# Optimization experiments

Measured on AMD Instinct MI355X. Metric: run time of the kernel, lower is better.

Reference implementation:

```python
import jax, jax.numpy as jnp
import numpy as np

EPS = 1e-5

def _conv(x, w, pad):
    # NCHW / OIHW 2-D convolution, stride 1
    return jax.lax.conv_general_dilated(
        x, w, window_strides=(1, 1), padding=[(pad, pad), (pad, pad)],
        dimension_numbers=('NCHW', 'OIHW', 'NCHW'))

def _bn2d(x, g, b, m, v):
    inv = g * jax.lax.rsqrt(v + EPS)
    return x * inv[None, :, None, None] + (b - m * inv)[None, :, None, None]

def _bn1d(x, g, b, m, v):
    inv = g * jax.lax.rsqrt(v + EPS)
    return x * inv[None, :] + (b - m * inv)[None, :]

def _avgpool2(x):
    B, C, H, W = x.shape
    return x.reshape(B, C, H // 2, 2, W // 2, 2).mean(axis=(3, 5))

def _hardtanh01(x):
    return jnp.clip(x, 0.0, 1.0)

def setup_inputs() -> dict:
    key = jax.random.key(0)
    ks = jax.random.split(key, 24)
    B = 1024
    d = {}
    d['x_in'] = jax.random.normal(ks[0], (B, 3, 32, 32), dtype=jnp.float32)
    d['w1'] = jax.random.normal(ks[1], (32, 3, 5, 5), dtype=jnp.float32) * 0.1
    d['w2'] = jax.random.normal(ks[2], (32, 32, 5, 5), dtype=jnp.float32) * 0.05
    d['w3'] = jax.random.normal(ks[3], (64, 32, 5, 5), dtype=jnp.float32) * 0.05
    d['w4'] = jax.random.normal(ks[4], (10, 64, 4, 4), dtype=jnp.float32) * 0.05
    for i, (c, k0) in enumerate([(32, 5), (32, 9), (64, 13), (10, 17)], start=1):
        d[f'g{i}'] = jax.random.uniform(ks[k0], (c,), minval=0.5, maxval=1.5, dtype=jnp.float32)
        d[f'b{i}'] = jax.random.normal(ks[k0 + 1], (c,), dtype=jnp.float32) * 0.1
        d[f'm{i}'] = jax.random.normal(ks[k0 + 2], (c,), dtype=jnp.float32) * 0.1
        d[f'v{i}'] = jax.random.uniform(ks[k0 + 3], (c,), minval=0.5, maxval=1.5, dtype=jnp.float32)
    return d

def reference(x_in, w1, w2, w3, w4,
              g1, b1, m1, v1, g2, b2, m2, v2,
              g3, b3, m3, v3, g4, b4, m4, v4):
    # conv1 -> bn1 -> pool -> hardtanh(0,1)
    x = _hardtanh01(_avgpool2(_bn2d(_conv(x_in, w1, 2), g1, b1, m1, v1)))
    # conv2 -> bn2 -> pool -> hardtanh(0,1)
    x = _hardtanh01(_avgpool2(_bn2d(_conv(x, w2, 2), g2, b2, m2, v2)))
    # conv3 -> bn3 -> pool -> hardtanh(0,1)
    x = _hardtanh01(_avgpool2(_bn2d(_conv(x, w3, 2), g3, b3, m3, v3)))
    # fc1 as 4x4 conv, valid padding -> (B, num_classes, 1, 1)
    x = _conv(x, w4, 0).reshape(x.shape[0], -1)
    return _bn1d(x, g4, b4, m4, v4)
```

## Files before the change

### kernel.cpp

```cpp
#include <hip/hip_runtime.h>

#define EPSF 1e-5f

typedef _Float16 half8 __attribute__((ext_vector_type(8)));
typedef _Float16 half4v __attribute__((ext_vector_type(4)));
typedef _Float16 half2v __attribute__((ext_vector_type(2)));
typedef float f32x4 __attribute__((ext_vector_type(4)));

__device__ __forceinline__ float clamp01(float x){ return fminf(fmaxf(x, 0.f), 1.f); }

__global__ __launch_bounds__(256) void k_prep(
    const float* __restrict__ w1, const float* __restrict__ w2,
    const float* __restrict__ w3, const float* __restrict__ w4,
    const float* __restrict__ g1, const float* __restrict__ b1, const float* __restrict__ m1, const float* __restrict__ v1,
    const float* __restrict__ g2, const float* __restrict__ b2, const float* __restrict__ m2, const float* __restrict__ v2,
    const float* __restrict__ g3, const float* __restrict__ b3, const float* __restrict__ m3, const float* __restrict__ v3,
    const float* __restrict__ g4, const float* __restrict__ b4, const float* __restrict__ m4, const float* __restrict__ v4,
    _Float16* __restrict__ w1h, _Float16* __restrict__ w2h, _Float16* __restrict__ w3h,
    _Float16* __restrict__ w4h, float* __restrict__ bnc)
{
  const int t = blockIdx.x*256 + threadIdx.x;
  if (t < 5120) {
    int c = t / 160, k = t - c*160;
    int oc = (c < 16) ? 2*c : 2*(c-16)+1;
    int dy = k >> 5, rem = k & 31, dx = rem >> 2, ic = rem & 3;
    float val = (dx < 5 && ic < 3) ? w1[(oc*3+ic)*25 + dy*5 + dx] : 0.f;
    w1h[t] = (_Float16)val;
  }
  for (int i = t; i < 25600; i += 32768) {
    int tap = i >> 10, r = i & 1023, c = r >> 5, ic = r & 31;
    int oc = (c < 16) ? 2*c : 2*(c-16)+1;
    w2h[i] = (_Float16)w2[(oc*32+ic)*25 + tap];
  }
  for (int i = t; i < 51200; i += 32768) {
    int tap = i >> 11, r = i & 2047, oc = r >> 5, ic = r & 31;
    w3h[i] = (_Float16)w3[(oc*32+ic)*25 + tap];
  }
  for (int i = t; i < 16384; i += 32768) {
    int oc = i >> 10, k = i & 1023, pos = k >> 6, ic = k & 63;
    float val = (oc < 10) ? w4[(oc*64+ic)*16 + pos] : 0.f;
    w4h[i] = (_Float16)val;
  }
  if (t < 32) {
    float inv = g1[t] / sqrtf(v1[t] + EPSF);
    bnc[t] = 0.25f*inv; bnc[32+t] = b1[t] - m1[t]*inv;
    float i2 = g2[t] / sqrtf(v2[t] + EPSF);
    bnc[64+t] = 0.25f*i2; bnc[96+t] = b2[t] - m2[t]*i2;
  }
  if (t < 64) {
    float i3 = g3[t] / sqrtf(v3[t] + EPSF);
    bnc[128+t] = 0.25f*i3; bnc[192+t] = b3[t] - m3[t]*i3;
  }
  if (t < 10) {
    float i4 = g4[t] / sqrtf(v4[t] + EPSF);
    bnc[256+t] = i4; bnc[266+t] = b4[t] - m4[t]*i4;
  }
}

__global__ __launch_bounds__(256, 4) void k_fused(
    const float* __restrict__ x,
    const _Float16* __restrict__ w1h, const _Float16* __restrict__ w2h,
    const _Float16* __restrict__ w3h, const _Float16* __restrict__ w4h,
    const float* __restrict__ bnc, float* __restrict__ out)
{
  __shared__ __align__(16) char arena[32000];
  _Float16* Bx1 = (_Float16*)arena;
  float*    Img = (float*)(arena + 11264);
  _Float16* P2  = (_Float16*)arena;
  _Float16* P3  = (_Float16*)arena;
  _Float16* Ip3 = (_Float16*)(arena + 11520);
  float*    S4P = (float*)(arena + 13568);

  const int img = blockIdx.x;
  const int tid = threadIdx.x;
  const int w   = __builtin_amdgcn_readfirstlane(tid >> 6);
  const int l   = tid & 63;
  const int row = l & 15;
  const int kg  = l >> 4;

  {
    const float4* src = (const float4*)(x + img*3072);
    float4* dst = (float4*)Img;
    dst[tid] = src[tid]; dst[tid+256] = src[tid+256]; dst[tid+512] = src[tid+512];
  }
  __syncthreads();

  for (int j = tid; j < 1400; j += 256) {
    int y = j / 40, xx = j - y*40;
    float s0 = 0.f, s1 = 0.f, s2 = 0.f;
    #pragma unroll
    for (int r = 0; r < 2; ++r) {
      int iy = y - 2 + r;
      if ((unsigned)iy < 32u) {
        #pragma unroll
        for (int cc = 0; cc < 2; ++cc) {
          int ix = xx - 2 + cc;
          if ((unsigned)ix < 32u) {
            const float* ip = Img + iy*32 + ix;
            s0 += ip[0]; s1 += ip[1024]; s2 += ip[2048];
          }
        }
      }
    }
    half4v h; h[0] = (_Float16)s0; h[1] = (_Float16)s1; h[2] = (_Float16)s2; h[3] = (_Float16)0.f;
    *(half4v*)(Bx1 + y*160 + xx*4) = h;
  }
  __syncthreads();

  f32x4 acc1[4][2];
  {
    half8 B1[5][2];
    #pragma unroll
    for (int dy = 0; dy < 5; ++dy) {
      B1[dy][0] = *(const half8*)(w1h + row*160 + dy*32 + kg*8);
      B1[dy][1] = *(const half8*)(w1h + (16 + row)*160 + dy*32 + kg*8);
    }
    #pragma unroll
    for (int mt = 0; mt < 4; ++mt) { acc1[mt][0] = (f32x4){0,0,0,0}; acc1[mt][1] = (f32x4){0,0,0,0}; }
    const int xoff = 8*(row + kg);
    #pragma unroll
    for (int mt = 0; mt < 4; ++mt) {
      const int py = w*4 + mt;
      #pragma unroll
      for (int dy = 0; dy < 5; ++dy) {
        half8 av = *(const half8*)(Bx1 + (2*py + dy)*160 + xoff);
        acc1[mt][0] = __builtin_amdgcn_mfma_f32_16x16x32_f16(av, B1[dy][0], acc1[mt][0], 0, 0, 0);
        acc1[mt][1] = __builtin_amdgcn_mfma_f32_16x16x32_f16(av, B1[dy][1], acc1[mt][1], 0, 0, 0);
      }
    }
  }
  __syncthreads();

  for (int j = tid; j < 1600; j += 256) {
    int u = j & 3, pos = j >> 2;
    int a = pos/20, c = pos - a*20;
    bool interior = ((unsigned)(a-2) < 16u) & ((unsigned)(c-2) < 16u);
    if (!interior) *(half8*)(P2 + pos*40 + u*8) = (half8)(_Float16)0.f;
  }
  {
    const int oce = 2*row;
    const float sA = bnc[oce],   hA = bnc[32 + oce];
    const float sB = bnc[oce+1], hB = bnc[32 + oce + 1];
    #pragma unroll
    for (int mt = 0; mt < 4; ++mt) {
      const int py = w*4 + mt;
      #pragma unroll
      for (int r = 0; r < 4; ++r) {
        int pcol = kg*4 + r;
        int idx = ((py+2)*20 + pcol+2)*40;
        half2v h;
        h[0] = (_Float16)clamp01(fmaf(acc1[mt][0][r], sA, hA));
        h[1] = (_Float16)clamp01(fmaf(acc1[mt][1][r], sB, hB));
        *(half2v*)(P2 + idx + oce) = h;
      }
    }
  }
  __syncthreads();

  f32x4 a2_0 = {0,0,0,0}, a2_1 = {0,0,0,0};
  {
    const int pixel = w*16 + row;
    const int py = pixel >> 3, px = pixel & 7;
    const _Float16* base = P2 + ((2*py)*20 + 2*px)*40 + kg*8;
    half8 RA[6], RB[6];
    #pragma unroll
    for (int c = 0; c < 6; ++c) RA[c] = *(const half8*)(base + c*40);
    #pragma unroll
    for (int c = 0; c < 6; ++c) RB[c] = *(const half8*)(base + 800 + c*40);
    const _Float16* wb = w2h + row*32 + kg*8;
    half8 cw0 = *(const half8*)(wb);
    half8 cw1 = *(const half8*)(wb + 512);
    #pragma unroll
    for (int dy = 0; dy < 5; ++dy) {
      half8 cs[6];
      #pragma unroll
      for (int c = 0; c < 6; ++c) cs[c] = RA[c] + RB[c];
      if (dy < 4) {
        #pragma unroll
        for (int c = 0; c < 6; ++c) {
          half8 nv = *(const half8*)(base + (dy+2)*800 + c*40);
          if ((dy & 1) == 0) RA[c] = nv; else RB[c] = nv;
        }
      }
      #pragma unroll
      for (int dx = 0; dx < 5; ++dx) {
        const int tap = dy*5 + dx;
        const int tn = (tap < 24) ? tap + 1 : 24;
        half8 nw0 = *(const half8*)(wb + tn*1024);
        half8 nw1 = *(const half8*)(wb + tn*1024 + 512);
        half8 av = cs[dx] + cs[dx+1];
        a2_0 = __builtin_amdgcn_mfma_f32_16x16x32_f16(av, cw0, a2_0, 0, 0, 0);
        a2_1 = __builtin_amdgcn_mfma_f32_16x16x32_f16(av, cw1, a2_1, 0, 0, 0);
        cw0 = nw0; cw1 = nw1;
      }
    }
  }
  __syncthreads();

  for (int j = tid; j < 576; j += 256) {
    int u = j & 3, pos = j >> 2;
    int a = pos/12, c = pos - a*12;
    bool interior = ((unsigned)(a-2) < 8u) & ((unsigned)(c-2) < 8u);
    if (!interior) *(half8*)(P3 + pos*40 + u*8) = (half8)(_Float16)0.f;
  }
  {
    const int oce = 2*row;
    const float sA = bnc[64 + oce],   hA = bnc[96 + oce];
    const float sB = bnc[64 + oce+1], hB = bnc[96 + oce + 1];
    #pragma unroll
    for (int r = 0; r < 4; ++r) {
      int p2 = w*16 + kg*4 + r;
      int py2 = p2 >> 3, px2 = p2 & 7;
      int idx = ((py2+2)*12 + px2+2)*40;
      half2v h;
      h[0] = (_Float16)clamp01(fmaf(a2_0[r], sA, hA));
      h[1] = (_Float16)clamp01(fmaf(a2_1[r], sB, hB));
      *(half2v*)(P3 + idx + oce) = h;
    }
  }
  __syncthreads();

  {
    const int py = row >> 2, px = row & 3;
    const _Float16* base = P3 + ((2*py)*12 + 2*px)*40 + kg*8;
    half8 RA[6], RB[6];
    #pragma unroll
    for (int c = 0; c < 6; ++c) RA[c] = *(const half8*)(base + c*40);
    #pragma unroll
    for (int c = 0; c < 6; ++c) RB[c] = *(const half8*)(base + 480 + c*40);
    const _Float16* wb = w3h + (w*16 + row)*32 + kg*8;
    half8 cw = *(const half8*)(wb);
    f32x4 a3 = {0,0,0,0};
    #pragma unroll
    for (int dy = 0; dy < 5; ++dy) {
      half8 cs[6];
      #pragma unroll
      for (int c = 0; c < 6; ++c) cs[c] = RA[c] + RB[c];
      if (dy < 4) {
        #pragma unroll
        for (int c = 0; c < 6; ++c) {
          half8 nv = *(const half8*)(base + (dy+2)*480 + c*40);
          if ((dy & 1) == 0) RA[c] = nv; else RB[c] = nv;
        }
      }
      #pragma unroll
      for (int dx = 0; dx < 5; ++dx) {
        const int tap = dy*5 + dx;
        const int tn = (tap < 24) ? tap + 1 : 24;
        half8 nw = *(const half8*)(wb + tn*2048);
        half8 av = cs[dx] + cs[dx+1];
        a3 = __builtin_amdgcn_mfma_f32_16x16x32_f16(av, cw, a3, 0, 0, 0);
        cw = nw;
      }
    }
    const int oc = w*16 + row;
    const float s3 = bnc[128 + oc], h3 = bnc[192 + oc];
    #pragma unroll
    for (int r = 0; r < 4; ++r)
      Ip3[(kg*4 + r)*64 + oc] = (_Float16)clamp01(fmaf(a3[r], s3, h3));
  }
  __syncthreads();

  if (tid < 160) {
    const int oc = tid >> 4, pix = tid & 15;
    const _Float16* A = Ip3 + pix*64;
    const _Float16* W = w4h + oc*1024 + pix*64;
    float a = 0.f;
    #pragma unroll
    for (int q = 0; q < 8; ++q) {
      half8 xa = *(const half8*)(A + q*8);
      half8 wv = *(const half8*)(W + q*8);
      #pragma unroll
      for (int j = 0; j < 8; ++j)
        a = fmaf((float)xa[j], (float)wv[j], a);
    }
    S4P[tid] = a;
  }
  __syncthreads();
  if (tid < 10) {
    float s = 0.f;
    #pragma unroll
    for (int i = 0; i < 16; ++i) s += S4P[tid*16 + i];
    out[img*10 + tid] = fmaf(s, bnc[256 + tid], bnc[266 + tid]);
  }
}

extern "C" void kernel_launch(void* const* d_in, const int* in_sizes, int n_in,
                              void* d_out, int out_size, void* d_ws, size_t ws_size,
                              hipStream_t stream)
{
  const float* x  = (const float*)d_in[0];
  const float* w1 = (const float*)d_in[1];
  const float* w2 = (const float*)d_in[2];
  const float* w3 = (const float*)d_in[3];
  const float* w4 = (const float*)d_in[4];
  const float *g1=(const float*)d_in[5],  *b1=(const float*)d_in[6],
              *m1=(const float*)d_in[7],  *v1=(const float*)d_in[8];
  const float *g2=(const float*)d_in[9],  *b2=(const float*)d_in[10],
              *m2=(const float*)d_in[11], *v2=(const float*)d_in[12];
  const float *g3=(const float*)d_in[13], *b3=(const float*)d_in[14],
              *m3=(const float*)d_in[15], *v3=(const float*)d_in[16];
  const float *g4=(const float*)d_in[17], *b4=(const float*)d_in[18],
              *m4=(const float*)d_in[19], *v4=(const float*)d_in[20];
  float* out = (float*)d_out;

  char* ws = (char*)d_ws;
  _Float16* w1h = (_Float16*)(ws);
  _Float16* w2h = (_Float16*)(ws + 10240);
  _Float16* w3h = (_Float16*)(ws + 61440);
  _Float16* w4h = (_Float16*)(ws + 163840);
  float*    bnc = (float*)   (ws + 196608);

  k_prep<<<dim3(128), dim3(256), 0, stream>>>(w1, w2, w3, w4,
      g1,b1,m1,v1, g2,b2,m2,v2, g3,b3,m3,v3, g4,b4,m4,v4,
      w1h, w2h, w3h, w4h, bnc);
  k_fused<<<dim3(1024), dim3(256), 0, stream>>>(x, w1h, w2h, w3h, w4h, bnc, out);
}
```

Measured before the change: 126.9 us.

## Split fused conv kernel across eight waves by output-channel halves

The block grows from 256 to 512 threads so the first two conv stages split work two ways across waves. Waves 0-3 and 4-7 each compute one half of the output channels, so each wave issues half the MFMAs and holds half the accumulators. Each wave now writes single fp16 values instead of packed half2 pairs. The third stage still runs only on the first four waves, so those waves are idle on the others while the block keeps more threads and LDS live per image.

```diff
diff --git a/kernel.cpp b/kernel.cpp
--- a/kernel.cpp
+++ b/kernel.cpp
@@ -4,7 +4,6 @@
 
 typedef _Float16 half8 __attribute__((ext_vector_type(8)));
 typedef _Float16 half4v __attribute__((ext_vector_type(4)));
-typedef _Float16 half2v __attribute__((ext_vector_type(2)));
 typedef float f32x4 __attribute__((ext_vector_type(4)));
 
 __device__ __forceinline__ float clamp01(float x){ return fminf(fmaxf(x, 0.f), 1.f); }
@@ -57,7 +56,7 @@
   }
 }
 
-__global__ __launch_bounds__(256, 4) void k_fused(
+__global__ __launch_bounds__(512, 6) void k_fused(
     const float* __restrict__ x,
     const _Float16* __restrict__ w1h, const _Float16* __restrict__ w2h,
     const _Float16* __restrict__ w3h, const _Float16* __restrict__ w4h,
@@ -77,15 +76,18 @@
   const int l   = tid & 63;
   const int row = l & 15;
   const int kg  = l >> 4;
+  const int mtb = w & 3;
+  const int ntb = w >> 2;
 
   {
     const float4* src = (const float4*)(x + img*3072);
     float4* dst = (float4*)Img;
-    dst[tid] = src[tid]; dst[tid+256] = src[tid+256]; dst[tid+512] = src[tid+512];
-  }
-  __syncthreads();
-
-  for (int j = tid; j < 1400; j += 256) {
+    dst[tid] = src[tid];
+    if (tid < 256) dst[tid + 512] = src[tid + 512];
+  }
+  __syncthreads();
+
+  for (int j = tid; j < 1400; j += 512) {
     int y = j / 40, xx = j - y*40;
     float s0 = 0.f, s1 = 0.f, s2 = 0.f;
     #pragma unroll
@@ -107,59 +109,52 @@
   }
   __syncthreads();
 
-  f32x4 acc1[4][2];
-  {
-    half8 B1[5][2];
-    #pragma unroll
-    for (int dy = 0; dy < 5; ++dy) {
-      B1[dy][0] = *(const half8*)(w1h + row*160 + dy*32 + kg*8);
-      B1[dy][1] = *(const half8*)(w1h + (16 + row)*160 + dy*32 + kg*8);
-    }
-    #pragma unroll
-    for (int mt = 0; mt < 4; ++mt) { acc1[mt][0] = (f32x4){0,0,0,0}; acc1[mt][1] = (f32x4){0,0,0,0}; }
+  f32x4 acc1[4];
+  {
+    half8 B1[5];
+    #pragma unroll
+    for (int dy = 0; dy < 5; ++dy)
+      B1[dy] = *(const half8*)(w1h + (ntb*16 + row)*160 + dy*32 + kg*8);
+    #pragma unroll
+    for (int mt = 0; mt < 4; ++mt) acc1[mt] = (f32x4){0,0,0,0};
     const int xoff = 8*(row + kg);
     #pragma unroll
     for (int mt = 0; mt < 4; ++mt) {
-      const int py = w*4 + mt;
+      const int py = mtb*4 + mt;
       #pragma unroll
       for (int dy = 0; dy < 5; ++dy) {
         half8 av = *(const half8*)(Bx1 + (2*py + dy)*160 + xoff);
-        acc1[mt][0] = __builtin_amdgcn_mfma_f32_16x16x32_f16(av, B1[dy][0], acc1[mt][0], 0, 0, 0);
-        acc1[mt][1] = __builtin_amdgcn_mfma_f32_16x16x32_f16(av, B1[dy][1], acc1[mt][1], 0, 0, 0);
-      }
-    }
-  }
-  __syncthreads();
-
-  for (int j = tid; j < 1600; j += 256) {
+        acc1[mt] = __builtin_amdgcn_mfma_f32_16x16x32_f16(av, B1[dy], acc1[mt], 0, 0, 0);
+      }
+    }
+  }
+  __syncthreads();
+
+  for (int j = tid; j < 1600; j += 512) {
     int u = j & 3, pos = j >> 2;
     int a = pos/20, c = pos - a*20;
     bool interior = ((unsigned)(a-2) < 16u) & ((unsigned)(c-2) < 16u);
     if (!interior) *(half8*)(P2 + pos*40 + u*8) = (half8)(_Float16)0.f;
   }
   {
-    const int oce = 2*row;
-    const float sA = bnc[oce],   hA = bnc[32 + oce];
-    const float sB = bnc[oce+1], hB = bnc[32 + oce + 1];
+    const int oc = 2*row + ntb;
+    const float sA = bnc[oc], hA = bnc[32 + oc];
     #pragma unroll
     for (int mt = 0; mt < 4; ++mt) {
-      const int py = w*4 + mt;
+      const int py = mtb*4 + mt;
       #pragma unroll
       for (int r = 0; r < 4; ++r) {
         int pcol = kg*4 + r;
         int idx = ((py+2)*20 + pcol+2)*40;
-        half2v h;
-        h[0] = (_Float16)clamp01(fmaf(acc1[mt][0][r], sA, hA));
-        h[1] = (_Float16)clamp01(fmaf(acc1[mt][1][r], sB, hB));
-        *(half2v*)(P2 + idx + oce) = h;
-      }
-    }
-  }
-  __syncthreads();
-
-  f32x4 a2_0 = {0,0,0,0}, a2_1 = {0,0,0,0};
-  {
-    const int pixel = w*16 + row;
+        P2[idx + oc] = (_Float16)clamp01(fmaf(acc1[mt][r], sA, hA));
+      }
+    }
+  }
+  __syncthreads();
+
+  f32x4 a2 = {0,0,0,0};
+  {
+    const int pixel = mtb*16 + row;
     const int py = pixel >> 3, px = pixel & 7;
     const _Float16* base = P2 + ((2*py)*20 + 2*px)*40 + kg*8;
     half8 RA[6], RB[6];
@@ -167,9 +162,8 @@
     for (int c = 0; c < 6; ++c) RA[c] = *(const half8*)(base + c*40);
     #pragma unroll
     for (int c = 0; c < 6; ++c) RB[c] = *(const half8*)(base + 800 + c*40);
-    const _Float16* wb = w2h + row*32 + kg*8;
-    half8 cw0 = *(const half8*)(wb);
-    half8 cw1 = *(const half8*)(wb + 512);
+    const _Float16* wb = w2h + (ntb*16 + row)*32 + kg*8;
+    half8 cw = *(const half8*)(wb);
     #pragma unroll
     for (int dy = 0; dy < 5; ++dy) {
       half8 cs[6];
@@ -186,41 +180,35 @@
       for (int dx = 0; dx < 5; ++dx) {
         const int tap = dy*5 + dx;
         const int tn = (tap < 24) ? tap + 1 : 24;
-        half8 nw0 = *(const half8*)(wb + tn*1024);
-        half8 nw1 = *(const half8*)(wb + tn*1024 + 512);
+        half8 nw = *(const half8*)(wb + tn*1024);
         half8 av = cs[dx] + cs[dx+1];
-        a2_0 = __builtin_amdgcn_mfma_f32_16x16x32_f16(av, cw0, a2_0, 0, 0, 0);
-        a2_1 = __builtin_amdgcn_mfma_f32_16x16x32_f16(av, cw1, a2_1, 0, 0, 0);
-        cw0 = nw0; cw1 = nw1;
-      }
-    }
-  }
-  __syncthreads();
-
-  for (int j = tid; j < 576; j += 256) {
+        a2 = __builtin_amdgcn_mfma_f32_16x16x32_f16(av, cw, a2, 0, 0, 0);
+        cw = nw;
+      }
+    }
+  }
+  __syncthreads();
+
+  for (int j = tid; j < 576; j += 512) {
     int u = j & 3, pos = j >> 2;
     int a = pos/12, c = pos - a*12;
     bool interior = ((unsigned)(a-2) < 8u) & ((unsigned)(c-2) < 8u);
     if (!interior) *(half8*)(P3 + pos*40 + u*8) = (half8)(_Float16)0.f;
   }
   {
-    const int oce = 2*row;
-    const float sA = bnc[64 + oce],   hA = bnc[96 + oce];
-    const float sB = bnc[64 + oce+1], hB = bnc[96 + oce + 1];
+    const int oc = 2*row + ntb;
+    const float sA = bnc[64 + oc], hA = bnc[96 + oc];
     #pragma unroll
     for (int r = 0; r < 4; ++r) {
-      int p2 = w*16 + kg*4 + r;
+      int p2 = mtb*16 + kg*4 + r;
       int py2 = p2 >> 3, px2 = p2 & 7;
       int idx = ((py2+2)*12 + px2+2)*40;
-      half2v h;
-      h[0] = (_Float16)clamp01(fmaf(a2_0[r], sA, hA));
-      h[1] = (_Float16)clamp01(fmaf(a2_1[r], sB, hB));
-      *(half2v*)(P3 + idx + oce) = h;
-    }
-  }
-  __syncthreads();
-
-  {
+      P3[idx + oc] = (_Float16)clamp01(fmaf(a2[r], sA, hA));
+    }
+  }
+  __syncthreads();
+
+  if (w < 4) {
     const int py = row >> 2, px = row & 3;
     const _Float16* base = P3 + ((2*py)*12 + 2*px)*40 + kg*8;
     half8 RA[6], RB[6];
@@ -314,5 +302,5 @@
   k_prep<<<dim3(128), dim3(256), 0, stream>>>(w1, w2, w3, w4,
       g1,b1,m1,v1, g2,b2,m2,v2, g3,b3,m3,v3, g4,b4,m4,v4,
       w1h, w2h, w3h, w4h, bnc);
-  k_fused<<<dim3(1024), dim3(256), 0, stream>>>(x, w1h, w2h, w3h, w4h, bnc, out);
+  k_fused<<<dim3(1024), dim3(512), 0, stream>>>(x, w1h, w2h, w3h, w4h, bnc, out);
 }
```

Result: slower. 129.8 us (+2.3%).
